# Performance work log

Measured on AMD Instinct MI355X. Metric: run time of the kernel, lower is better.

Reference implementation:

```python
import jax, jax.numpy as jnp
import numpy as np

N, E = 50000, 800000
D_IN_N, D_IN_E, D_OUT = 64, 64, 64


def setup_inputs() -> dict:
    key = jax.random.key(0)
    ks = jax.random.split(key, 10)
    stdv = 1.0 / np.sqrt(D_OUT)
    u = lambda k, shape: jax.random.uniform(k, shape, jnp.float32, -stdv, stdv)
    return {
        "nf": jax.random.normal(ks[0], (N, D_IN_N), jnp.float32),
        "ef": jax.random.normal(ks[1], (E, D_IN_E), jnp.float32),
        "src": jax.random.randint(ks[2], (E,), 0, N, jnp.int32),
        "dst": jax.random.randint(ks[3], (E,), 0, N, jnp.int32),
        "W_node": u(ks[4], (D_IN_N, D_OUT)),
        "W_edge": u(ks[5], (D_IN_E, D_OUT)),
        "bias_node": u(ks[6], (D_OUT,)),
        "bias_edge": u(ks[7], (D_OUT,)),
        "W_dense": u(ks[8], (2 * D_OUT, D_OUT)),  # Linear(2*out, out) weight, stored transposed
        "b_dense": u(ks[9], (D_OUT,)),
    }


def reference(nf, ef, src, dst, W_node, W_edge, bias_node, bias_edge, W_dense, b_dense):
    n_nodes = nf.shape[0]
    # input projections
    nf_h = nf @ W_node                     # [N, D]
    ef_h = ef @ W_edge                     # [E, D]
    # update_all: mean of incoming edge features per dst node (0 for isolated nodes, DGL default)
    deg = jax.ops.segment_sum(jnp.ones((ef_h.shape[0],), ef_h.dtype), dst, num_segments=n_nodes)
    nb_ef = jax.ops.segment_sum(ef_h, dst, num_segments=n_nodes) / jnp.maximum(deg, 1.0)[:, None]
    # apply_nodes: nf = act(nf + bias)
    nf_out = jax.nn.relu(nf_h + bias_node)
    # apply_edges (uses updated nf): cat([ef + nb_ef[dst], (nf[src]+nf[dst])/2]) -> Linear -> +bias -> act
    tmp_ef = ef_h + nb_ef[dst]             # [E, D]
    srcdst_nf = (nf_out[src] + nf_out[dst]) * 0.5
    ef_out = jnp.concatenate([tmp_ef, srcdst_nf], axis=1) @ W_dense + b_dense + bias_edge
    ef_out = jax.nn.relu(ef_out)
    return nf_out, ef_out
```

## Files before the change

### kernel.cpp

```cpp
#include <hip/hip_runtime.h>

#define D 64

typedef __attribute__((ext_vector_type(8))) short short8;
typedef __attribute__((ext_vector_type(4))) float f32x4;

__device__ __forceinline__ ushort f2b(float f) {
    union { float f; unsigned u; } x; x.f = f;
    unsigned r = x.u + 0x7FFFu + ((x.u >> 16) & 1u);
    return (ushort)(r >> 16);
}
__device__ __forceinline__ float b2f(ushort u) {
    union { float f; unsigned u; } x; x.u = ((unsigned)u) << 16;
    return x.f;
}
__device__ __forceinline__ short8 pack8(float4 a, float4 b) {
    short8 r;
    r[0] = (short)f2b(a.x); r[1] = (short)f2b(a.y); r[2] = (short)f2b(a.z); r[3] = (short)f2b(a.w);
    r[4] = (short)f2b(b.x); r[5] = (short)f2b(b.y); r[6] = (short)f2b(b.z); r[7] = (short)f2b(b.w);
    return r;
}

__global__ __launch_bounds__(256) void fused_front_kernel(
    const float* __restrict__ nf, const float* __restrict__ Wn,
    const float* __restrict__ bias, const float* __restrict__ Wd,
    float* __restrict__ out, ushort* __restrict__ nfp_b, int N,
    const int* __restrict__ dst, int* __restrict__ deg_i, int E,
    const float* __restrict__ W_edge, const float* __restrict__ b_dense,
    const float* __restrict__ bias_edge, ushort* __restrict__ Wcomb_b,
    float* __restrict__ bias2, int NPB, int HB)
{
    __shared__ float Ws[D * D];
    __shared__ float Wb[D * D];
    __shared__ float As[16 * D];
    __shared__ float Vs[16 * D];
    const int tid = threadIdx.x;
    const int bid = blockIdx.x;

    if (bid < NPB) {
        constexpr int ROWS = 16;
        const long row0 = (long)bid * ROWS;
        const float* Wd_bot = Wd + D * D;
        #pragma unroll
        for (int i = tid; i < D * D / 4; i += 256) {
            ((float4*)Ws)[i] = ((const float4*)Wn)[i];
            float4 v = ((const float4*)Wd_bot)[i];
            ((float4*)Wb)[i] = make_float4(0.5f * v.x, 0.5f * v.y, 0.5f * v.z, 0.5f * v.w);
        }
        {
            int i = tid;
            long r = row0 + (i * 4) / D;
            ((float4*)As)[i] = (r < N) ? ((const float4*)nf)[row0 * D / 4 + i]
                                       : make_float4(0.f, 0.f, 0.f, 0.f);
        }
        __syncthreads();

        const int c = tid & 63;
        const float b = bias[c];
        for (int rr = tid >> 6; rr < ROWS; rr += 4) {
            float acc = 0.f;
            #pragma unroll
            for (int k = 0; k < D; ++k)
                acc = fmaf(As[rr * D + k], Ws[k * D + c], acc);
            float v = fmaxf(acc + b, 0.f);
            Vs[rr * D + c] = v;
            long r = row0 + rr;
            if (r < N) out[r * D + c] = v;
        }
        __syncthreads();
        for (int rr = tid >> 6; rr < ROWS; rr += 4) {
            float acc = 0.f;
            #pragma unroll
            for (int k = 0; k < D; ++k)
                acc = fmaf(Vs[rr * D + k], Wb[k * D + c], acc);
            long r = row0 + rr;
            if (r < N) nfp_b[r * D + c] = f2b(acc);
        }
    } else if (bid < NPB + HB) {
        int i = (bid - NPB) * 256 + tid;
        if (i < E) atomicAdd(deg_i + dst[i], 1);
    } else {
        for (int idx = tid; idx < D * D; idx += 256) {
            int k = idx >> 6, n = idx & 63;
            float s = 0.f;
            #pragma unroll 8
            for (int j = 0; j < D; ++j)
                s = fmaf(W_edge[k * D + j], Wd[j * D + n], s);
            Wcomb_b[n * D + k] = f2b(s);
        }
        if (tid < D) bias2[tid] = b_dense[tid] + bias_edge[tid];
    }
}

__global__ __launch_bounds__(256) void scanA_kernel(
    const int* __restrict__ deg_i, int* __restrict__ pos,
    int* __restrict__ bsum, int N)
{
    __shared__ int s[256];
    const int tid = threadIdx.x;
    const int i = blockIdx.x * 256 + tid;
    int v = (i < N) ? deg_i[i] : 0;
    s[tid] = v;
    __syncthreads();
    #pragma unroll
    for (int off = 1; off < 256; off <<= 1) {
        int t = (tid >= off) ? s[tid - off] : 0;
        __syncthreads();
        s[tid] += t;
        __syncthreads();
    }
    if (i < N) pos[i] = s[tid] - v;
    if (tid == 255) bsum[blockIdx.x] = s[255];
}

__global__ __launch_bounds__(256) void scanB_kernel(int* __restrict__ bsum, int NB)
{
    __shared__ int s[256];
    const int tid = threadIdx.x;
    int v = (tid < NB) ? bsum[tid] : 0;
    s[tid] = v;
    __syncthreads();
    #pragma unroll
    for (int off = 1; off < 256; off <<= 1) {
        int t = (tid >= off) ? s[tid - off] : 0;
        __syncthreads();
        s[tid] += t;
        __syncthreads();
    }
    if (tid < NB) bsum[tid] = s[tid] - v;
}

__global__ __launch_bounds__(256) void scanC_kernel(
    const int* __restrict__ pos, int* __restrict__ cursor,
    const int* __restrict__ bsum, int N)
{
    int i = blockIdx.x * 256 + threadIdx.x;
    if (i < N) cursor[i] = pos[i] + bsum[blockIdx.x];
}

__global__ __launch_bounds__(256) void scatter_kernel(
    const int* __restrict__ dst, int* __restrict__ cursor,
    int2* __restrict__ sorted_ed, int E)
{
    int i = blockIdx.x * 256 + threadIdx.x;
    if (i < E) {
        int dv = dst[i];
        int slot = atomicAdd(cursor + dv, 1);
        sorted_ed[slot] = make_int2(i, dv);
    }
}

#define SEG_ROWS 256
#define SLSTR 34
__global__ __launch_bounds__(256) void efp_seg_kernel(
    const float* __restrict__ ef, const int2* __restrict__ sorted_ed,
    const ushort* __restrict__ Wt, ushort* __restrict__ efp,
    float* __restrict__ nb_sum, int E)
{
    __shared__ unsigned Slds[SEG_ROWS * SLSTR];
    __shared__ int dsts[SEG_ROWS];
    const int tid = threadIdx.x;
    const long s0 = (long)blockIdx.x * SEG_ROWS;

    const int w = tid >> 6, lane = tid & 63;
    const int lr = lane & 15, g = lane >> 4;
    const bool odd = lane & 1;

    long gde[4];
    #pragma unroll
    for (int tt = 0; tt < 4; ++tt) {
        long s = s0 + 64 * tt + 16 * w + lr;
        if (s >= E) s = E - 1;
        gde[tt] = (long)sorted_ed[s].x;
    }
    float4 va[4][4];
    #pragma unroll
    for (int tt = 0; tt < 4; ++tt) {
        const float4* ap = (const float4*)(ef + gde[tt] * D);
        va[tt][0] = ap[2 * g];     va[tt][1] = ap[2 * g + 1];
        va[tt][2] = ap[8 + 2 * g]; va[tt][3] = ap[8 + 2 * g + 1];
    }
    int rbl[4]; long seo[4][2];
    #pragma unroll
    for (int tt = 0; tt < 4; ++tt) {
        rbl[tt] = 64 * tt + 16 * w + 4 * g + (odd ? 2 : 0);
        long s = s0 + rbl[tt];
        if (s > E - 2) s = (E - 2) & ~1L;
        int4 q = *(const int4*)&sorted_ed[s];
        seo[tt][0] = (long)q.x * D;
        seo[tt][1] = (long)q.z * D;
    }
    {
        long s = s0 + tid;
        dsts[tid] = (s < E) ? sorted_ed[s].y : -1;
    }

    short8 bf0[4], bf1[4];
    #pragma unroll
    for (int t = 0; t < 4; ++t) {
        bf0[t] = *(const short8*)&Wt[(16 * t + lr) * D + 8 * g];
        bf1[t] = *(const short8*)&Wt[(16 * t + lr) * D + 32 + 8 * g];
    }

    #pragma unroll
    for (int tt = 0; tt < 4; ++tt) {
        short8 a0 = pack8(va[tt][0], va[tt][1]);
        short8 a1 = pack8(va[tt][2], va[tt][3]);
        f32x4 acc[4];
        #pragma unroll
        for (int t = 0; t < 4; ++t) {
            f32x4 z = {0.f, 0.f, 0.f, 0.f};
            z = __builtin_amdgcn_mfma_f32_16x16x32_bf16(a0, bf0[t], z, 0, 0, 0);
            z = __builtin_amdgcn_mfma_f32_16x16x32_bf16(a1, bf1[t], z, 0, 0, 0);
            acc[t] = z;
        }

        const int rb = rbl[tt];
        long sl0 = s0 + rb, sl1 = s0 + rb + 1;
        #pragma unroll
        for (int t = 0; t < 4; ++t) {
            float p0 = __shfl_xor(acc[t][0], 1, 64);
            float p1 = __shfl_xor(acc[t][1], 1, 64);
            float p2 = __shfl_xor(acc[t][2], 1, 64);
            float p3 = __shfl_xor(acc[t][3], 1, 64);
            float lo0, hi0, lo1, hi1;
            if (odd) { lo0 = p2; hi0 = acc[t][2]; lo1 = p3; hi1 = acc[t][3]; }
            else     { lo0 = acc[t][0]; hi0 = p0; lo1 = acc[t][1]; hi1 = p1; }
            int cbase = 16 * t + (lr & ~1);
            int dc = cbase >> 1;
            unsigned dw0 = ((unsigned)f2b(hi0) << 16) | (unsigned)f2b(lo0);
            unsigned dw1 = ((unsigned)f2b(hi1) << 16) | (unsigned)f2b(lo1);
            if (sl0 < E) *(unsigned*)(efp + seo[tt][0] + cbase) = dw0;
            if (sl1 < E) *(unsigned*)(efp + seo[tt][1] + cbase) = dw1;
            Slds[rb * SLSTR + dc]       = dw0;
            Slds[(rb + 1) * SLSTR + dc] = dw1;
        }
    }
    __syncthreads();

    {
        const int dwc = tid & 31;
        const int r0 = (tid >> 5) * 32;
        float seg0 = 0.f, seg1 = 0.f;
        int cur = dsts[r0];
        #pragma unroll 4
        for (int r = r0; r < r0 + 32; ++r) {
            int dv = dsts[r];
            unsigned u = Slds[r * SLSTR + dwc];
            if (dv != cur) {
                if (cur >= 0) {
                    atomicAdd(nb_sum + (long)cur * D + 2 * dwc, seg0);
                    atomicAdd(nb_sum + (long)cur * D + 2 * dwc + 1, seg1);
                }
                seg0 = seg1 = 0.f;
                cur = dv;
            }
            seg0 += b2f((ushort)(u & 0xffff));
            seg1 += b2f((ushort)(u >> 16));
        }
        if (cur >= 0) {
            atomicAdd(nb_sum + (long)cur * D + 2 * dwc, seg0);
            atomicAdd(nb_sum + (long)cur * D + 2 * dwc + 1, seg1);
        }
    }
}

__global__ __launch_bounds__(256) void ndp_lite_kernel(
    const float* __restrict__ nb_sum, const int* __restrict__ deg_i,
    const ushort* __restrict__ nfp_b, ushort* __restrict__ ndp_b, int N)
{
    long i = (long)blockIdx.x * 256 + threadIdx.x;
    long node = i >> 3;
    int cb = (int)(i & 7);
    if (node >= N) return;
    float inv = 1.0f / fmaxf((float)deg_i[node], 1.0f);
    const float4* sp = (const float4*)(nb_sum + node * D + cb * 8);
    float4 x0 = sp[0], x1 = sp[1];
    short8 np = *(const short8*)(nfp_b + node * D + cb * 8);
    short8 r;
    r[0] = (short)f2b(x0.x * inv + b2f((ushort)np[0]));
    r[1] = (short)f2b(x0.y * inv + b2f((ushort)np[1]));
    r[2] = (short)f2b(x0.z * inv + b2f((ushort)np[2]));
    r[3] = (short)f2b(x0.w * inv + b2f((ushort)np[3]));
    r[4] = (short)f2b(x1.x * inv + b2f((ushort)np[4]));
    r[5] = (short)f2b(x1.y * inv + b2f((ushort)np[5]));
    r[6] = (short)f2b(x1.z * inv + b2f((ushort)np[6]));
    r[7] = (short)f2b(x1.w * inv + b2f((ushort)np[7]));
    *(short8*)(ndp_b + node * D + cb * 8) = r;
}

__global__ __launch_bounds__(256) void final_kernel(
    const ushort* __restrict__ efp, const int* __restrict__ src,
    const int* __restrict__ dst, const ushort* __restrict__ ndp_b,
    const ushort* __restrict__ nfp_b, const float* __restrict__ bias2,
    float* __restrict__ out, int E)
{
    long idx = (long)blockIdx.x * 256 + threadIdx.x;
    long e = idx >> 2;
    int q = (int)(idx & 3);
    if (e >= E) return;
    int dv = dst[e], sv = src[e];
    const short8* ep = (const short8*)(efp + e * D + q * 16);
    const short8* np = (const short8*)(ndp_b + (long)dv * D + q * 16);
    const short8* sp = (const short8*)(nfp_b + (long)sv * D + q * 16);
    short8 e0 = ep[0], e1 = ep[1];
    short8 n0 = np[0], n1 = np[1];
    short8 s0 = sp[0], s1 = sp[1];
    const float4* bp = (const float4*)(bias2 + q * 16);
    float4 b0 = bp[0], b1 = bp[1], b2 = bp[2], b3 = bp[3];

    float r[16];
    #pragma unroll
    for (int j = 0; j < 8; ++j) {
        r[j]     = b2f((ushort)e0[j]) + b2f((ushort)n0[j]) + b2f((ushort)s0[j]);
        r[8 + j] = b2f((ushort)e1[j]) + b2f((ushort)n1[j]) + b2f((ushort)s1[j]);
    }
    float4* op = (float4*)(out + e * D + q * 16);
    op[0] = make_float4(fmaxf(r[0] + b0.x, 0.f), fmaxf(r[1] + b0.y, 0.f),
                        fmaxf(r[2] + b0.z, 0.f), fmaxf(r[3] + b0.w, 0.f));
    op[1] = make_float4(fmaxf(r[4] + b1.x, 0.f), fmaxf(r[5] + b1.y, 0.f),
                        fmaxf(r[6] + b1.z, 0.f), fmaxf(r[7] + b1.w, 0.f));
    op[2] = make_float4(fmaxf(r[8] + b2.x, 0.f), fmaxf(r[9] + b2.y, 0.f),
                        fmaxf(r[10] + b2.z, 0.f), fmaxf(r[11] + b2.w, 0.f));
    op[3] = make_float4(fmaxf(r[12] + b3.x, 0.f), fmaxf(r[13] + b3.y, 0.f),
                        fmaxf(r[14] + b3.z, 0.f), fmaxf(r[15] + b3.w, 0.f));
}

extern "C" void kernel_launch(void* const* d_in, const int* in_sizes, int n_in,
                              void* d_out, int out_size, void* d_ws, size_t ws_size,
                              hipStream_t stream) {
    const float* nf        = (const float*)d_in[0];
    const float* ef        = (const float*)d_in[1];
    const int*   src       = (const int*)d_in[2];
    const int*   dst       = (const int*)d_in[3];
    const float* W_node    = (const float*)d_in[4];
    const float* W_edge    = (const float*)d_in[5];
    const float* bias_node = (const float*)d_in[6];
    const float* bias_edge = (const float*)d_in[7];
    const float* W_dense   = (const float*)d_in[8];
    const float* b_dense   = (const float*)d_in[9];

    const int N = in_sizes[0] / D;
    const int E = in_sizes[1] / D;
    const int NB = (N + 255) / 256;
    const int NPB = (N + 15) / 16;
    const int HB = (E + 255) / 256;

    float* nf_out = (float*)d_out;
    float* ef_out = (float*)d_out + (size_t)N * D;

    char* p = (char*)d_ws;
    int*    deg_i    = (int*)p;     p += (size_t)N * 4;
    float*  nb_sum   = (float*)p;   p += (size_t)N * D * 4;
    size_t  zbytes   = (size_t)(p - (char*)d_ws);
    int*    pos      = (int*)p;     p += (size_t)N * 4;
    int*    cursor   = (int*)p;     p += (size_t)N * 4;
    int*    bsum     = (int*)p;     p += 256 * 4;
    int2*   sorted_ed= (int2*)p;    p += (size_t)E * 8;
    ushort* nfp_b    = (ushort*)p;  p += (size_t)N * D * 2;
    ushort* ndp_b    = (ushort*)p;  p += (size_t)N * D * 2;
    ushort* Wcomb_b  = (ushort*)p;  p += D * D * 2;
    float*  bias2    = (float*)p;   p += 256;
    ushort* efp      = (ushort*)p;

    hipMemsetAsync(d_ws, 0, zbytes, stream);

    fused_front_kernel<<<NPB + HB + 1, 256, 0, stream>>>(
        nf, W_node, bias_node, W_dense, nf_out, nfp_b, N,
        dst, deg_i, E, W_edge, b_dense, bias_edge, Wcomb_b, bias2, NPB, HB);
    scanA_kernel<<<NB, 256, 0, stream>>>(deg_i, pos, bsum, N);
    scanB_kernel<<<1, 256, 0, stream>>>(bsum, NB);
    scanC_kernel<<<NB, 256, 0, stream>>>(pos, cursor, bsum, N);
    scatter_kernel<<<(E + 255) / 256, 256, 0, stream>>>(dst, cursor, sorted_ed, E);
    efp_seg_kernel<<<(E + SEG_ROWS - 1) / SEG_ROWS, 256, 0, stream>>>(
        ef, sorted_ed, Wcomb_b, efp, nb_sum, E);
    ndp_lite_kernel<<<(int)(((size_t)N * 8 + 255) / 256), 256, 0, stream>>>(
        nb_sum, deg_i, nfp_b, ndp_b, N);
    final_kernel<<<(int)(((size_t)E * 4 + 255) / 256), 256, 0, stream>>>(
        efp, src, dst, ndp_b, nfp_b, bias2, ef_out, E);
}
```

Measured before the change: 379.4 us.

## Use bf16 MFMA for node projection chain with 64-row tiles

Replaces the scalar fp32 FMA loops in the node-projection branch of the front kernel with bf16 MFMA 16x16x32 instructions. Weights are stored transposed in padded shared memory, and each block now handles 64 rows instead of 16. Output pairs are packed with lane shuffles so each write is a 32-bit store. This cuts the per-block weight staging and the scalar compute cost, but rounds the node projection inputs to bf16, which lowers precision of nf_out.

```diff
diff --git a/kernel.cpp b/kernel.cpp
--- a/kernel.cpp
+++ b/kernel.cpp
@@ -20,6 +20,8 @@
     r[4] = (short)f2b(b.x); r[5] = (short)f2b(b.y); r[6] = (short)f2b(b.z); r[7] = (short)f2b(b.w);
     return r;
 }
+
+#define LDA 72
 
 __global__ __launch_bounds__(256) void fused_front_kernel(
     const float* __restrict__ nf, const float* __restrict__ Wn,
@@ -30,51 +32,94 @@
     const float* __restrict__ bias_edge, ushort* __restrict__ Wcomb_b,
     float* __restrict__ bias2, int NPB, int HB)
 {
-    __shared__ float Ws[D * D];
-    __shared__ float Wb[D * D];
-    __shared__ float As[16 * D];
-    __shared__ float Vs[16 * D];
+    __shared__ ushort Bn[64 * LDA];
+    __shared__ ushort Bd[64 * LDA];
+    __shared__ ushort Vs[64 * LDA];
     const int tid = threadIdx.x;
     const int bid = blockIdx.x;
 
     if (bid < NPB) {
-        constexpr int ROWS = 16;
-        const long row0 = (long)bid * ROWS;
-        const float* Wd_bot = Wd + D * D;
-        #pragma unroll
-        for (int i = tid; i < D * D / 4; i += 256) {
-            ((float4*)Ws)[i] = ((const float4*)Wn)[i];
-            float4 v = ((const float4*)Wd_bot)[i];
-            ((float4*)Wb)[i] = make_float4(0.5f * v.x, 0.5f * v.y, 0.5f * v.z, 0.5f * v.w);
-        }
+        const long row0 = (long)bid * 64;
+        const int w = tid >> 6, lane = tid & 63;
+        const int lr = lane & 15, g = lane >> 4;
+        const bool odd = lane & 1;
+
         {
-            int i = tid;
-            long r = row0 + (i * 4) / D;
-            ((float4*)As)[i] = (r < N) ? ((const float4*)nf)[row0 * D / 4 + i]
-                                       : make_float4(0.f, 0.f, 0.f, 0.f);
-        }
-        __syncthreads();
-
-        const int c = tid & 63;
-        const float b = bias[c];
-        for (int rr = tid >> 6; rr < ROWS; rr += 4) {
-            float acc = 0.f;
+            int k = tid >> 2, n0 = (tid & 3) * 16;
+            const float4* wr = (const float4*)(Wn + (long)k * D + n0);
+            float4 v0 = wr[0], v1 = wr[1], v2 = wr[2], v3 = wr[3];
+            float vs[16] = {v0.x, v0.y, v0.z, v0.w, v1.x, v1.y, v1.z, v1.w,
+                            v2.x, v2.y, v2.z, v2.w, v3.x, v3.y, v3.z, v3.w};
             #pragma unroll
-            for (int k = 0; k < D; ++k)
-                acc = fmaf(As[rr * D + k], Ws[k * D + c], acc);
-            float v = fmaxf(acc + b, 0.f);
-            Vs[rr * D + c] = v;
-            long r = row0 + rr;
-            if (r < N) out[r * D + c] = v;
-        }
-        __syncthreads();
-        for (int rr = tid >> 6; rr < ROWS; rr += 4) {
-            float acc = 0.f;
+            for (int j = 0; j < 16; ++j) Bn[(n0 + j) * LDA + k] = f2b(vs[j]);
+            const float4* wd = (const float4*)(Wd + (long)(D + k) * D + n0);
+            float4 u0 = wd[0], u1 = wd[1], u2 = wd[2], u3 = wd[3];
+            float us[16] = {u0.x, u0.y, u0.z, u0.w, u1.x, u1.y, u1.z, u1.w,
+                            u2.x, u2.y, u2.z, u2.w, u3.x, u3.y, u3.z, u3.w};
             #pragma unroll
-            for (int k = 0; k < D; ++k)
-                acc = fmaf(Vs[rr * D + k], Wb[k * D + c], acc);
-            long r = row0 + rr;
-            if (r < N) nfp_b[r * D + c] = f2b(acc);
+            for (int j = 0; j < 16; ++j) Bd[(n0 + j) * LDA + k] = f2b(0.5f * us[j]);
+        }
+
+        long era = row0 + 16 * w + lr; if (era >= N) era = N - 1;
+        const float4* ap = (const float4*)(nf + era * D);
+        float4 v0 = ap[2 * g], v1 = ap[2 * g + 1];
+        float4 v2 = ap[8 + 2 * g], v3 = ap[8 + 2 * g + 1];
+        short8 a0 = pack8(v0, v1), a1 = pack8(v2, v3);
+        __syncthreads();
+
+        f32x4 acc[4];
+        #pragma unroll
+        for (int t = 0; t < 4; ++t) {
+            f32x4 z = {0.f, 0.f, 0.f, 0.f};
+            short8 b0 = *(const short8*)&Bn[(16 * t + lr) * LDA + 8 * g];
+            short8 b1 = *(const short8*)&Bn[(16 * t + lr) * LDA + 32 + 8 * g];
+            z = __builtin_amdgcn_mfma_f32_16x16x32_bf16(a0, b0, z, 0, 0, 0);
+            z = __builtin_amdgcn_mfma_f32_16x16x32_bf16(a1, b1, z, 0, 0, 0);
+            acc[t] = z;
+        }
+        #pragma unroll
+        for (int t = 0; t < 4; ++t) {
+            int c = 16 * t + lr;
+            float bb = bias[c];
+            #pragma unroll
+            for (int reg = 0; reg < 4; ++reg) {
+                int r = 16 * w + 4 * g + reg;
+                float v = fmaxf(acc[t][reg] + bb, 0.f);
+                long rg = row0 + r;
+                if (rg < N) out[rg * D + c] = v;
+                Vs[r * LDA + c] = f2b(v);
+            }
+        }
+        __syncthreads();
+
+        short8 c0 = *(const short8*)&Vs[(16 * w + lr) * LDA + 8 * g];
+        short8 c1 = *(const short8*)&Vs[(16 * w + lr) * LDA + 32 + 8 * g];
+        f32x4 acc2[4];
+        #pragma unroll
+        for (int t = 0; t < 4; ++t) {
+            f32x4 z = {0.f, 0.f, 0.f, 0.f};
+            short8 b0 = *(const short8*)&Bd[(16 * t + lr) * LDA + 8 * g];
+            short8 b1 = *(const short8*)&Bd[(16 * t + lr) * LDA + 32 + 8 * g];
+            z = __builtin_amdgcn_mfma_f32_16x16x32_bf16(c0, b0, z, 0, 0, 0);
+            z = __builtin_amdgcn_mfma_f32_16x16x32_bf16(c1, b1, z, 0, 0, 0);
+            acc2[t] = z;
+        }
+        const int rb = 16 * w + 4 * g + (odd ? 2 : 0);
+        long e0 = row0 + rb, e1 = row0 + rb + 1;
+        #pragma unroll
+        for (int t = 0; t < 4; ++t) {
+            float p0 = __shfl_xor(acc2[t][0], 1, 64);
+            float p1 = __shfl_xor(acc2[t][1], 1, 64);
+            float p2 = __shfl_xor(acc2[t][2], 1, 64);
+            float p3 = __shfl_xor(acc2[t][3], 1, 64);
+            float lo0, hi0, lo1, hi1;
+            if (odd) { lo0 = p2; hi0 = acc2[t][2]; lo1 = p3; hi1 = acc2[t][3]; }
+            else     { lo0 = acc2[t][0]; hi0 = p0; lo1 = acc2[t][1]; hi1 = p1; }
+            int cbase = 16 * t + (lr & ~1);
+            unsigned dw0 = ((unsigned)f2b(hi0) << 16) | (unsigned)f2b(lo0);
+            unsigned dw1 = ((unsigned)f2b(hi1) << 16) | (unsigned)f2b(lo1);
+            if (e0 < N) *(unsigned*)(nfp_b + e0 * D + cbase) = dw0;
+            if (e1 < N) *(unsigned*)(nfp_b + e1 * D + cbase) = dw1;
         }
     } else if (bid < NPB + HB) {
         int i = (bid - NPB) * 256 + tid;
@@ -343,7 +388,7 @@
     const int N = in_sizes[0] / D;
     const int E = in_sizes[1] / D;
     const int NB = (N + 255) / 256;
-    const int NPB = (N + 15) / 16;
+    const int NPB = (N + 63) / 64;
     const int HB = (E + 255) / 256;
 
     float* nf_out = (float*)d_out;
```

Result: faster. 358.4 us (-5.5%).
